# Kernel optimization log

Hardware: AMD Instinct MI355X
Metric: run time of the kernel (lower is better)

The kernel has to match this reference:

```python
import jax, jax.numpy as jnp
import numpy as np

B, S, D = 4, 2048, 768
H = 12
HD = D // H  # 64
EPS = 1e-12  # F.normalize eps


def setup_inputs() -> dict:
    key = jax.random.key(0)
    ks = jax.random.split(key, 6)
    scale = 1.0 / np.sqrt(D)
    x = jax.random.normal(ks[0], (B, S, D), dtype=jnp.float32)
    Wq = jax.random.normal(ks[1], (D, D), dtype=jnp.float32) * scale
    Wk = jax.random.normal(ks[2], (D, D), dtype=jnp.float32) * scale
    Wv = jax.random.normal(ks[3], (D, D), dtype=jnp.float32) * scale
    Wo = jax.random.normal(ks[4], (D, D), dtype=jnp.float32) * scale
    temperature = jnp.ones((H, 1, 1), dtype=jnp.float32)
    return {"x": x, "Wq": Wq, "Wk": Wk, "Wv": Wv, "Wo": Wo, "temperature": temperature}


def _heads(t):
    # [B,S,D] -> [B,H,S,HD]
    return t.reshape(B, S, H, HD).transpose(0, 2, 1, 3)


def reference(x, Wq, Wk, Wv, Wo, temperature):
    # Linear weights stored torch-style [out,in]: y = x @ W.T
    q = _heads(x @ Wq.T)
    k = _heads(x @ Wk.T)
    v = _heads(x @ Wv.T)
    # cosine-sim normalize (F.normalize: x / max(||x||, eps))
    q = q / jnp.maximum(jnp.linalg.norm(q, axis=-1, keepdims=True), EPS)
    k = k / jnp.maximum(jnp.linalg.norm(k, axis=-1, keepdims=True), EPS)
    # [B,H,S,S] scores with per-head learnable temperature
    attn = jnp.einsum("bhqd,bhkd->bhqk", q, k) * temperature  # temperature broadcasts [H,1,1]
    causal = jnp.tril(jnp.ones((S, S), dtype=bool))
    attn = jnp.where(causal, attn, -jnp.inf)
    attn = jax.nn.softmax(attn, axis=-1)
    out = jnp.einsum("bhqk,bhkd->bhqd", attn, v)
    out = out.transpose(0, 2, 1, 3).reshape(B, S, D)
    return out @ Wo.T
```

## Files before the change

### kernel.cpp

```cpp
#include <hip/hip_runtime.h>
#include <hip/hip_bf16.h>

#define B_ 4
#define S_ 2048
#define D_ 768
#define H_ 12
#define HD_ 64
#define M_ (B_*S_)
#define LOG2E 1.44269504088896f

typedef __attribute__((ext_vector_type(8))) short bf8;
typedef __attribute__((ext_vector_type(4))) float f4;
typedef unsigned short u16;
typedef unsigned int   u32;

__device__ __forceinline__ float bf2f(u16 u) {
  union { u32 i; float f; } c; c.i = ((u32)u) << 16; return c.f;
}
__device__ __forceinline__ u16 f2bf(float x) {
  union { float f; u32 i; } c; c.f = x;
  u32 r = (c.i + 0x7FFFu + ((c.i >> 16) & 1u)) >> 16;
  return (u16)r;
}
__device__ __forceinline__ u16 cvt_bf16(float x) {
  u32 r;
  asm("v_cvt_pk_bf16_f32 %0, %1, %1" : "=v"(r) : "v"(x));
  return (u16)r;
}
__device__ __forceinline__ float exp2_raw(float x) {
  float r;
  asm("v_exp_f32 %0, %1" : "=v"(r) : "v"(x));
  return r;
}

__global__ __launch_bounds__(256) void stage_cvt(const float* __restrict__ in,
                                                 u16* __restrict__ out, int n4)
{
  for (int i = blockIdx.x * blockDim.x + threadIdx.x; i < n4; i += gridDim.x * blockDim.x) {
    float4 v = ((const float4*)in)[i];
    ushort4 o;
    o.x = f2bf(v.x); o.y = f2bf(v.y); o.z = f2bf(v.z); o.w = f2bf(v.w);
    ((ushort4*)out)[i] = o;
  }
}

__global__ __launch_bounds__(256) void stage_w4(const float* __restrict__ w0, const float* __restrict__ w1,
                                                const float* __restrict__ w2, const float* __restrict__ w3,
                                                u16* __restrict__ o0, u16* __restrict__ o1,
                                                u16* __restrict__ o2, u16* __restrict__ o3, int n4)
{
  const float* src = (blockIdx.y == 0) ? w0 : (blockIdx.y == 1) ? w1 : (blockIdx.y == 2) ? w2 : w3;
  u16*         dst = (blockIdx.y == 0) ? o0 : (blockIdx.y == 1) ? o1 : (blockIdx.y == 2) ? o2 : o3;
  for (int i = blockIdx.x * blockDim.x + threadIdx.x; i < n4; i += gridDim.x * blockDim.x) {
    float4 v = ((const float4*)src)[i];
    ushort4 o;
    o.x = f2bf(v.x); o.y = f2bf(v.y); o.z = f2bf(v.z); o.w = f2bf(v.w);
    ((ushort4*)dst)[i] = o;
  }
}

__device__ __forceinline__ bf8 ldcvt8(const float* __restrict__ p) {
  float4 a = *(const float4*)p;
  float4 b = *(const float4*)(p + 4);
  bf8 r;
  r[0] = f2bf(a.x); r[1] = f2bf(a.y); r[2] = f2bf(a.z); r[3] = f2bf(a.w);
  r[4] = f2bf(b.x); r[5] = f2bf(b.y); r[6] = f2bf(b.z); r[7] = f2bf(b.w);
  return r;
}

#define MFMA_BF16 __builtin_amdgcn_mfma_f32_16x16x32_bf16

template <int EPI>
__global__ __launch_bounds__(256) void gemm_v2(const u16* __restrict__ A,
                                               const u16* __restrict__ W,
                                               u16* __restrict__ Cb,
                                               float* __restrict__ Cf,
                                               const float* __restrict__ temp)
{
  const int w  = threadIdx.x >> 6;
  const int ln = threadIdx.x & 63;
  const int li = ln & 15, g = ln >> 4;
  const int wr = w >> 1, wc = w & 1;
  const int row0 = blockIdx.x * 64;
  const int col0 = blockIdx.y * 128;

  __shared__ __align__(16) u16 a_lds[64][72];
  __shared__ __align__(16) u16 b_lds[128][72];

  const int rowA = threadIdx.x >> 2;
  const int cA   = (threadIdx.x & 3) * 8;
  const int rowB = threadIdx.x >> 1;
  const int cB   = (threadIdx.x & 1) * 32;

  const u16* Asrc = A + (size_t)(row0 + rowA) * 768 + cA;
  const u16* Bsrc = W + (size_t)(col0 + rowB) * 768 + cB;

  bf8 ra0 = *(const bf8*)(Asrc);
  bf8 ra1 = *(const bf8*)(Asrc + 32);
  bf8 rb0 = *(const bf8*)(Bsrc);
  bf8 rb1 = *(const bf8*)(Bsrc + 8);
  bf8 rb2 = *(const bf8*)(Bsrc + 16);
  bf8 rb3 = *(const bf8*)(Bsrc + 24);

  f4 acc[2][4];
#pragma unroll
  for (int i = 0; i < 2; ++i)
#pragma unroll
    for (int j = 0; j < 4; ++j) acc[i][j] = (f4){0.f, 0.f, 0.f, 0.f};

  for (int kt = 0; kt < 12; ++kt) {
    __syncthreads();
    *(bf8*)&a_lds[rowA][cA]      = ra0;
    *(bf8*)&a_lds[rowA][cA + 32] = ra1;
    *(bf8*)&b_lds[rowB][cB]      = rb0;
    *(bf8*)&b_lds[rowB][cB + 8]  = rb1;
    *(bf8*)&b_lds[rowB][cB + 16] = rb2;
    *(bf8*)&b_lds[rowB][cB + 24] = rb3;
    if (kt < 11) {
      const u16* as = Asrc + (kt + 1) * 64;
      const u16* bs = Bsrc + (kt + 1) * 64;
      ra0 = *(const bf8*)(as);
      ra1 = *(const bf8*)(as + 32);
      rb0 = *(const bf8*)(bs);
      rb1 = *(const bf8*)(bs + 8);
      rb2 = *(const bf8*)(bs + 16);
      rb3 = *(const bf8*)(bs + 24);
    }
    asm volatile("s_waitcnt lgkmcnt(0)" ::: "memory");
    __builtin_amdgcn_s_barrier();

#pragma unroll
    for (int kk = 0; kk < 2; ++kk) {
      bf8 a0 = *(const bf8*)&a_lds[wr * 32 + li][kk * 32 + g * 8];
      bf8 a1 = *(const bf8*)&a_lds[wr * 32 + 16 + li][kk * 32 + g * 8];
      bf8 b0 = *(const bf8*)&b_lds[wc * 64 + li][kk * 32 + g * 8];
      bf8 b1 = *(const bf8*)&b_lds[wc * 64 + 16 + li][kk * 32 + g * 8];
      bf8 b2 = *(const bf8*)&b_lds[wc * 64 + 32 + li][kk * 32 + g * 8];
      bf8 b3 = *(const bf8*)&b_lds[wc * 64 + 48 + li][kk * 32 + g * 8];
      acc[0][0] = MFMA_BF16(a0, b0, acc[0][0], 0, 0, 0);
      acc[0][1] = MFMA_BF16(a0, b1, acc[0][1], 0, 0, 0);
      acc[0][2] = MFMA_BF16(a0, b2, acc[0][2], 0, 0, 0);
      acc[0][3] = MFMA_BF16(a0, b3, acc[0][3], 0, 0, 0);
      acc[1][0] = MFMA_BF16(a1, b0, acc[1][0], 0, 0, 0);
      acc[1][1] = MFMA_BF16(a1, b1, acc[1][1], 0, 0, 0);
      acc[1][2] = MFMA_BF16(a1, b2, acc[1][2], 0, 0, 0);
      acc[1][3] = MFMA_BF16(a1, b3, acc[1][3], 0, 0, 0);
    }
  }

  const int wrow0 = row0 + wr * 32;
  const int wcol0 = col0 + wc * 64;

  if (EPI == 1 || EPI == 2) {
    float tmul = 1.0f;
    if (EPI == 2) tmul = temp[wcol0 >> 6] * LOG2E;
#pragma unroll
    for (int i = 0; i < 2; ++i)
#pragma unroll
      for (int r = 0; r < 4; ++r) {
        float ss = 0.f;
#pragma unroll
        for (int j = 0; j < 4; ++j) ss += acc[i][j][r] * acc[i][j][r];
#pragma unroll
        for (int msk = 1; msk < 16; msk <<= 1) ss += __shfl_xor(ss, msk, 64);
        float scl = tmul / fmaxf(sqrtf(ss), 1e-12f);
#pragma unroll
        for (int j = 0; j < 4; ++j) acc[i][j][r] *= scl;
      }
  }

#pragma unroll
  for (int i = 0; i < 2; ++i)
#pragma unroll
    for (int j = 0; j < 4; ++j)
#pragma unroll
      for (int r = 0; r < 4; ++r) {
        int row = wrow0 + i * 16 + g * 4 + r;
        int col = wcol0 + j * 16 + li;
        if (EPI == 3) Cf[(size_t)row * 768 + col] = acc[i][j][r];
        else          Cb[(size_t)row * 768 + col] = f2bf(acc[i][j][r]);
      }
}

template <int EPI>
__global__ __launch_bounds__(256) void gemm_wf32(const u16* __restrict__ A,
                                                 const float* __restrict__ W,
                                                 u16* __restrict__ Cb,
                                                 float* __restrict__ Cf,
                                                 const float* __restrict__ temp)
{
  const int w  = threadIdx.x >> 6;
  const int ln = threadIdx.x & 63;
  const int li = ln & 15, g = ln >> 4;
  const int wr = w >> 1, wc = w & 1;
  const int row0 = blockIdx.x * 64 + wr * 32;
  const int col0 = blockIdx.y * 128 + wc * 64;

  const u16*   Ap = A + (size_t)(row0 + li) * 768 + g * 8;
  const float* Wp = W + (size_t)(col0 + li) * 768 + g * 8;

  f4 acc[2][4];
#pragma unroll
  for (int i = 0; i < 2; ++i)
#pragma unroll
    for (int j = 0; j < 4; ++j) acc[i][j] = (f4){0.f, 0.f, 0.f, 0.f};

  for (int k = 0; k < 768; k += 32) {
    bf8 a0 = *(const bf8*)(Ap + k);
    bf8 a1 = *(const bf8*)(Ap + (size_t)16 * 768 + k);
    bf8 b0 = ldcvt8(Wp + k);
    bf8 b1 = ldcvt8(Wp + (size_t)16 * 768 + k);
    bf8 b2 = ldcvt8(Wp + (size_t)32 * 768 + k);
    bf8 b3 = ldcvt8(Wp + (size_t)48 * 768 + k);
    acc[0][0] = MFMA_BF16(a0, b0, acc[0][0], 0, 0, 0);
    acc[0][1] = MFMA_BF16(a0, b1, acc[0][1], 0, 0, 0);
    acc[0][2] = MFMA_BF16(a0, b2, acc[0][2], 0, 0, 0);
    acc[0][3] = MFMA_BF16(a0, b3, acc[0][3], 0, 0, 0);
    acc[1][0] = MFMA_BF16(a1, b0, acc[1][0], 0, 0, 0);
    acc[1][1] = MFMA_BF16(a1, b1, acc[1][1], 0, 0, 0);
    acc[1][2] = MFMA_BF16(a1, b2, acc[1][2], 0, 0, 0);
    acc[1][3] = MFMA_BF16(a1, b3, acc[1][3], 0, 0, 0);
  }

  if (EPI == 1 || EPI == 2) {
    float tmul = 1.0f;
    if (EPI == 2) tmul = temp[col0 >> 6] * LOG2E;
#pragma unroll
    for (int i = 0; i < 2; ++i)
#pragma unroll
      for (int r = 0; r < 4; ++r) {
        float ss = 0.f;
#pragma unroll
        for (int j = 0; j < 4; ++j) ss += acc[i][j][r] * acc[i][j][r];
#pragma unroll
        for (int msk = 1; msk < 16; msk <<= 1) ss += __shfl_xor(ss, msk, 64);
        float scl = tmul / fmaxf(sqrtf(ss), 1e-12f);
#pragma unroll
        for (int j = 0; j < 4; ++j) acc[i][j][r] *= scl;
      }
  }

#pragma unroll
  for (int i = 0; i < 2; ++i)
#pragma unroll
    for (int j = 0; j < 4; ++j)
#pragma unroll
      for (int r = 0; r < 4; ++r) {
        int row = row0 + i * 16 + g * 4 + r;
        int col = col0 + j * 16 + li;
        if (EPI == 3) Cf[(size_t)row * 768 + col] = acc[i][j][r];
        else          Cb[(size_t)row * 768 + col] = f2bf(acc[i][j][r]);
      }
}

__global__ __launch_bounds__(256, 4) void flash_attn(const u16* __restrict__ Q,
                                                     const u16* __restrict__ K,
                                                     const u16* __restrict__ V,
                                                     u16* __restrict__ O,
                                                     const float* __restrict__ temp)
{
  const int bid = blockIdx.x;
  const int vid = (bid & 7) * 192 + (bid >> 3);
  const int bh  = vid >> 5;
  const int qt  = 31 - (vid & 31);
  const int b = bh / H_, h = bh % H_;
  const size_t base = (size_t)b * S_ * D_ + h * HD_;
  const u16* Qp = Q + base;
  const u16* Kp = K + base;
  const u16* Vp = V + base;
  u16*       Op = O + base;

  const float C2 = fabsf(temp[h]) * LOG2E;

  const int w  = threadIdx.x >> 6;
  const int ln = threadIdx.x & 63;
  const int li = ln & 15, g = ln >> 4;

  __shared__ __align__(16) u16 k_lds[64][72];
  __shared__ __align__(16) u16 vt[64][72];
  __shared__ __align__(16) u16 p_lds[4][16][72];

  const int q0 = qt * 64;
  const int qrow = q0 + w * 16 + li;

  bf8 qf0 = *(const bf8*)(Qp + (size_t)qrow * D_ + g * 8);
  bf8 qf1 = *(const bf8*)(Qp + (size_t)qrow * D_ + 32 + g * 8);

  const int key2 = (threadIdx.x >> 3) * 2;
  const int d0   = (threadIdx.x & 7) * 8;
  const u16* ksrc = Kp + (size_t)key2 * D_ + d0;
  const u16* vsrc = Vp + (size_t)key2 * D_ + d0;

  bf8 ka = *(const bf8*)(ksrc);
  bf8 kb = *(const bf8*)(ksrc + D_);
  bf8 va = *(const bf8*)(vsrc);
  bf8 vb_ = *(const bf8*)(vsrc + D_);

  f4 o[4];
  float lp[4] = {0.f, 0.f, 0.f, 0.f};
#pragma unroll
  for (int c = 0; c < 4; ++c) o[c] = (f4){0.f, 0.f, 0.f, 0.f};

  for (int kt = 0; kt <= qt; ++kt) {
    __syncthreads();
    {
      *(bf8*)&k_lds[key2][d0]     = ka;
      *(bf8*)&k_lds[key2 + 1][d0] = kb;
#pragma unroll
      for (int j = 0; j < 8; ++j) {
        ushort2 pr;
        pr.x = (u16)va[j]; pr.y = (u16)vb_[j];
        *(ushort2*)&vt[d0 + j][key2 ^ d0] = pr;
      }
    }
    if (kt < qt) {
      const u16* ks = ksrc + (size_t)(kt + 1) * 64 * D_;
      const u16* vs = vsrc + (size_t)(kt + 1) * 64 * D_;
      ka  = *(const bf8*)(ks);
      kb  = *(const bf8*)(ks + D_);
      va  = *(const bf8*)(vs);
      vb_ = *(const bf8*)(vs + D_);
    }
    asm volatile("s_waitcnt lgkmcnt(0)" ::: "memory");
    __builtin_amdgcn_s_barrier();

    f4 sc[4];
#pragma unroll
    for (int c = 0; c < 4; ++c) sc[c] = (f4){0.f, 0.f, 0.f, 0.f};
#pragma unroll
    for (int c = 0; c < 4; ++c) {
      bf8 k0 = *(const bf8*)&k_lds[c * 16 + li][g * 8];
      bf8 k1 = *(const bf8*)&k_lds[c * 16 + li][32 + g * 8];
      sc[c] = MFMA_BF16(qf0, k0, sc[c], 0, 0, 0);
      sc[c] = MFMA_BF16(qf1, k1, sc[c], 0, 0, 0);
    }

    if (kt == qt) {
#pragma unroll
      for (int c = 0; c < 4; ++c)
#pragma unroll
        for (int r = 0; r < 4; ++r) {
          int col = kt * 64 + c * 16 + li;
          int row = q0 + w * 16 + g * 4 + r;
          if (col > row) sc[c][r] = -__builtin_inff();
        }
    }

#pragma unroll
    for (int c = 0; c < 4; ++c)
#pragma unroll
      for (int r = 0; r < 4; ++r) {
        float p = exp2_raw(sc[c][r] - C2);
        sc[c][r] = p;
        lp[r] += p;
      }

#pragma unroll
    for (int c = 0; c < 4; ++c)
#pragma unroll
      for (int r = 0; r < 4; ++r)
        p_lds[w][g * 4 + r][(c * 16 + li) ^ (g << 3)] = cvt_bf16(sc[c][r]);

#pragma unroll
    for (int ks = 0; ks < 2; ++ks) {
      bf8 pa = *(const bf8*)&p_lds[w][li][(ks * 32 + g * 8) ^ ((li >> 2) << 3)];
#pragma unroll
      for (int c = 0; c < 4; ++c) {
        int d  = c * 16 + li;
        int kbx = (ks * 32 + g * 8) ^ (d & 56);
        bf8 vv = *(const bf8*)&vt[d][kbx];
        o[c] = MFMA_BF16(pa, vv, o[c], 0, 0, 0);
      }
    }
  }

  float l[4];
#pragma unroll
  for (int r = 0; r < 4; ++r) {
    float s = lp[r];
#pragma unroll
    for (int msk = 1; msk < 16; msk <<= 1) s += __shfl_xor(s, msk, 64);
    l[r] = 1.0f / s;
  }
#pragma unroll
  for (int c = 0; c < 4; ++c)
#pragma unroll
    for (int r = 0; r < 4; ++r) {
      int row = q0 + w * 16 + g * 4 + r;
      Op[(size_t)row * D_ + c * 16 + li] = cvt_bf16(o[c][r] * l[r]);
    }
}

extern "C" void kernel_launch(void* const* d_in, const int* in_sizes, int n_in,
                              void* d_out, int out_size, void* d_ws, size_t ws_size,
                              hipStream_t stream) {
  const void *xv, *Wqv, *Wkv, *Wvv, *Wov, *tv;
  if (in_sizes[0] == M_ * D_) {
    xv = d_in[0]; Wqv = d_in[1]; Wkv = d_in[2]; Wvv = d_in[3]; Wov = d_in[4]; tv = d_in[5];
  } else {
    Wkv = d_in[0]; Wov = d_in[1]; Wqv = d_in[2]; Wvv = d_in[3]; tv = d_in[4]; xv = d_in[5];
  }
  const float* x    = (const float*)xv;
  const float* Wq   = (const float*)Wqv;
  const float* Wk   = (const float*)Wkv;
  const float* Wv   = (const float*)Wvv;
  const float* Wo   = (const float*)Wov;
  const float* temp = (const float*)tv;

  const size_t SZ  = (size_t)M_ * D_;
  const size_t WSZ = (size_t)D_ * D_;
  u16* ws = (u16*)d_ws;
  u16* Qb = ws;
  u16* Kb = ws + SZ;
  u16* Vb = ws + 2 * SZ;
  u16* XB = (u16*)d_out;

  const bool stageW = ws_size >= (3 * SZ + 4 * WSZ) * sizeof(u16);
  u16* Wqb = ws + 3 * SZ;
  u16* Wkb = Wqb + WSZ;
  u16* Wvb = Wkb + WSZ;
  u16* Wob = Wvb + WSZ;

  stage_cvt<<<2048, 256, 0, stream>>>(x, XB, (int)(SZ / 4));

  dim3 gg(M_ / 64, D_ / 128), bb(256);
  if (stageW) {
    stage_w4<<<dim3(192, 4), 256, 0, stream>>>(Wq, Wk, Wv, Wo, Wqb, Wkb, Wvb, Wob, (int)(WSZ / 4));
    gemm_v2<2><<<gg, bb, 0, stream>>>(XB, Wqb, Qb, nullptr, temp);
    gemm_v2<1><<<gg, bb, 0, stream>>>(XB, Wkb, Kb, nullptr, temp);
    gemm_v2<0><<<gg, bb, 0, stream>>>(XB, Wvb, Vb, nullptr, temp);
  } else {
    gemm_wf32<2><<<gg, bb, 0, stream>>>(XB, Wq, Qb, nullptr, temp);
    gemm_wf32<1><<<gg, bb, 0, stream>>>(XB, Wk, Kb, nullptr, temp);
    gemm_wf32<0><<<gg, bb, 0, stream>>>(XB, Wv, Vb, nullptr, temp);
  }

  flash_attn<<<1536, 256, 0, stream>>>(Qb, Kb, Vb, Qb, temp);

  if (stageW) gemm_v2<3><<<gg, bb, 0, stream>>>(Qb, Wob, nullptr, (float*)d_out, temp);
  else        gemm_wf32<3><<<gg, bb, 0, stream>>>(Qb, Wo, nullptr, (float*)d_out, temp);
}
```

Measured before the change: 154.2 us.

## Use direct global-to-LDS loads with XOR swizzle and merge stage/QKV launches

```diff
diff --git a/kernel.cpp b/kernel.cpp
--- a/kernel.cpp
+++ b/kernel.cpp
@@ -14,6 +14,9 @@
 typedef unsigned short u16;
 typedef unsigned int   u32;
 
+typedef __attribute__((address_space(3))) u32 lds_u32;
+typedef __attribute__((address_space(1))) const u32 glob_u32;
+
 __device__ __forceinline__ float bf2f(u16 u) {
   union { u32 i; float f; } c; c.i = ((u32)u) << 16; return c.f;
 }
@@ -31,6 +34,29 @@
   float r;
   asm("v_exp_f32 %0, %1" : "=v"(r) : "v"(x));
   return r;
+}
+__device__ __forceinline__ void glds16(const u16* g, u16* l) {
+  __builtin_amdgcn_global_load_lds((glob_u32*)g, (lds_u32*)l, 16, 0, 0);
+}
+
+__global__ __launch_bounds__(256) void stage_all(const float* __restrict__ x,
+                                                 const float* __restrict__ w0, const float* __restrict__ w1,
+                                                 const float* __restrict__ w2, const float* __restrict__ w3,
+                                                 u16* __restrict__ xo,
+                                                 u16* __restrict__ o0, u16* __restrict__ o1,
+                                                 u16* __restrict__ o2, u16* __restrict__ o3,
+                                                 int nx4, int nw4)
+{
+  int y = blockIdx.y;
+  const float* src = (y == 0) ? x : (y == 1) ? w0 : (y == 2) ? w1 : (y == 3) ? w2 : w3;
+  u16*         dst = (y == 0) ? xo : (y == 1) ? o0 : (y == 2) ? o1 : (y == 3) ? o2 : o3;
+  int n4 = (y == 0) ? nx4 : nw4;
+  for (int i = blockIdx.x * blockDim.x + threadIdx.x; i < n4; i += gridDim.x * blockDim.x) {
+    float4 v = ((const float4*)src)[i];
+    ushort4 o;
+    o.x = f2bf(v.x); o.y = f2bf(v.y); o.z = f2bf(v.z); o.w = f2bf(v.w);
+    ((ushort4*)dst)[i] = o;
+  }
 }
 
 __global__ __launch_bounds__(256) void stage_cvt(const float* __restrict__ in,
@@ -41,21 +67,6 @@
     ushort4 o;
     o.x = f2bf(v.x); o.y = f2bf(v.y); o.z = f2bf(v.z); o.w = f2bf(v.w);
     ((ushort4*)out)[i] = o;
-  }
-}
-
-__global__ __launch_bounds__(256) void stage_w4(const float* __restrict__ w0, const float* __restrict__ w1,
-                                                const float* __restrict__ w2, const float* __restrict__ w3,
-                                                u16* __restrict__ o0, u16* __restrict__ o1,
-                                                u16* __restrict__ o2, u16* __restrict__ o3, int n4)
-{
-  const float* src = (blockIdx.y == 0) ? w0 : (blockIdx.y == 1) ? w1 : (blockIdx.y == 2) ? w2 : w3;
-  u16*         dst = (blockIdx.y == 0) ? o0 : (blockIdx.y == 1) ? o1 : (blockIdx.y == 2) ? o2 : o3;
-  for (int i = blockIdx.x * blockDim.x + threadIdx.x; i < n4; i += gridDim.x * blockDim.x) {
-    float4 v = ((const float4*)src)[i];
-    ushort4 o;
-    o.x = f2bf(v.x); o.y = f2bf(v.y); o.z = f2bf(v.z); o.w = f2bf(v.w);
-    ((ushort4*)dst)[i] = o;
   }
 }
 
@@ -71,11 +82,12 @@
 #define MFMA_BF16 __builtin_amdgcn_mfma_f32_16x16x32_bf16
 
 template <int EPI>
-__global__ __launch_bounds__(256) void gemm_v2(const u16* __restrict__ A,
-                                               const u16* __restrict__ W,
-                                               u16* __restrict__ Cb,
-                                               float* __restrict__ Cf,
-                                               const float* __restrict__ temp)
+__device__ __forceinline__ void gemm_core(u16* a_lds, u16* b_lds,
+                                          const u16* __restrict__ A,
+                                          const u16* __restrict__ W,
+                                          u16* __restrict__ Cb,
+                                          float* __restrict__ Cf,
+                                          const float* __restrict__ temp)
 {
   const int w  = threadIdx.x >> 6;
   const int ln = threadIdx.x & 63;
@@ -84,23 +96,10 @@
   const int row0 = blockIdx.x * 64;
   const int col0 = blockIdx.y * 128;
 
-  __shared__ __align__(16) u16 a_lds[64][72];
-  __shared__ __align__(16) u16 b_lds[128][72];
-
-  const int rowA = threadIdx.x >> 2;
-  const int cA   = (threadIdx.x & 3) * 8;
-  const int rowB = threadIdx.x >> 1;
-  const int cB   = (threadIdx.x & 1) * 32;
-
-  const u16* Asrc = A + (size_t)(row0 + rowA) * 768 + cA;
-  const u16* Bsrc = W + (size_t)(col0 + rowB) * 768 + cB;
-
-  bf8 ra0 = *(const bf8*)(Asrc);
-  bf8 ra1 = *(const bf8*)(Asrc + 32);
-  bf8 rb0 = *(const bf8*)(Bsrc);
-  bf8 rb1 = *(const bf8*)(Bsrc + 8);
-  bf8 rb2 = *(const bf8*)(Bsrc + 16);
-  bf8 rb3 = *(const bf8*)(Bsrc + 24);
+  const int srow = ln >> 3;
+  const int scol = ((ln & 7) ^ srow) * 8;
+  const u16* Abase = A + (size_t)(row0 + srow) * 768 + scol;
+  const u16* Bbase = W + (size_t)(col0 + srow) * 768 + scol;
 
   f4 acc[2][4];
 #pragma unroll
@@ -109,34 +108,29 @@
     for (int j = 0; j < 4; ++j) acc[i][j] = (f4){0.f, 0.f, 0.f, 0.f};
 
   for (int kt = 0; kt < 12; ++kt) {
+    const int k0 = kt * 64;
+#pragma unroll
+    for (int i = 0; i < 2; ++i) {
+      int seg = w * 2 + i;
+      glds16(Abase + (size_t)(seg * 8) * 768 + k0, a_lds + seg * 512);
+    }
+#pragma unroll
+    for (int i = 0; i < 4; ++i) {
+      int seg = w * 4 + i;
+      glds16(Bbase + (size_t)(seg * 8) * 768 + k0, b_lds + seg * 512);
+    }
+    asm volatile("s_waitcnt vmcnt(0)" ::: "memory");
     __syncthreads();
-    *(bf8*)&a_lds[rowA][cA]      = ra0;
-    *(bf8*)&a_lds[rowA][cA + 32] = ra1;
-    *(bf8*)&b_lds[rowB][cB]      = rb0;
-    *(bf8*)&b_lds[rowB][cB + 8]  = rb1;
-    *(bf8*)&b_lds[rowB][cB + 16] = rb2;
-    *(bf8*)&b_lds[rowB][cB + 24] = rb3;
-    if (kt < 11) {
-      const u16* as = Asrc + (kt + 1) * 64;
-      const u16* bs = Bsrc + (kt + 1) * 64;
-      ra0 = *(const bf8*)(as);
-      ra1 = *(const bf8*)(as + 32);
-      rb0 = *(const bf8*)(bs);
-      rb1 = *(const bf8*)(bs + 8);
-      rb2 = *(const bf8*)(bs + 16);
-      rb3 = *(const bf8*)(bs + 24);
-    }
-    asm volatile("s_waitcnt lgkmcnt(0)" ::: "memory");
-    __builtin_amdgcn_s_barrier();
 
 #pragma unroll
     for (int kk = 0; kk < 2; ++kk) {
-      bf8 a0 = *(const bf8*)&a_lds[wr * 32 + li][kk * 32 + g * 8];
-      bf8 a1 = *(const bf8*)&a_lds[wr * 32 + 16 + li][kk * 32 + g * 8];
-      bf8 b0 = *(const bf8*)&b_lds[wc * 64 + li][kk * 32 + g * 8];
-      bf8 b1 = *(const bf8*)&b_lds[wc * 64 + 16 + li][kk * 32 + g * 8];
-      bf8 b2 = *(const bf8*)&b_lds[wc * 64 + 32 + li][kk * 32 + g * 8];
-      bf8 b3 = *(const bf8*)&b_lds[wc * 64 + 48 + li][kk * 32 + g * 8];
+      const int co = (((kk * 4 + g) ^ (li & 7)) * 8);
+      bf8 a0 = *(const bf8*)(a_lds + (wr * 32 + li) * 64 + co);
+      bf8 a1 = *(const bf8*)(a_lds + (wr * 32 + 16 + li) * 64 + co);
+      bf8 b0 = *(const bf8*)(b_lds + (wc * 64 + li) * 64 + co);
+      bf8 b1 = *(const bf8*)(b_lds + (wc * 64 + 16 + li) * 64 + co);
+      bf8 b2 = *(const bf8*)(b_lds + (wc * 64 + 32 + li) * 64 + co);
+      bf8 b3 = *(const bf8*)(b_lds + (wc * 64 + 48 + li) * 64 + co);
       acc[0][0] = MFMA_BF16(a0, b0, acc[0][0], 0, 0, 0);
       acc[0][1] = MFMA_BF16(a0, b1, acc[0][1], 0, 0, 0);
       acc[0][2] = MFMA_BF16(a0, b2, acc[0][2], 0, 0, 0);
@@ -146,6 +140,7 @@
       acc[1][2] = MFMA_BF16(a1, b2, acc[1][2], 0, 0, 0);
       acc[1][3] = MFMA_BF16(a1, b3, acc[1][3], 0, 0, 0);
     }
+    __syncthreads();
   }
 
   const int wrow0 = row0 + wr * 32;
@@ -180,6 +175,29 @@
         if (EPI == 3) Cf[(size_t)row * 768 + col] = acc[i][j][r];
         else          Cb[(size_t)row * 768 + col] = f2bf(acc[i][j][r]);
       }
+}
+
+__global__ __launch_bounds__(256) void gemm_qkv(const u16* __restrict__ XB,
+                                                const u16* __restrict__ Wq, const u16* __restrict__ Wk,
+                                                const u16* __restrict__ Wv,
+                                                u16* __restrict__ Qb, u16* __restrict__ Kb,
+                                                u16* __restrict__ Vb,
+                                                const float* __restrict__ temp)
+{
+  __shared__ __align__(16) u16 a_lds[64 * 64];
+  __shared__ __align__(16) u16 b_lds[128 * 64];
+  if (blockIdx.z == 0)      gemm_core<2>(a_lds, b_lds, XB, Wq, Qb, nullptr, temp);
+  else if (blockIdx.z == 1) gemm_core<1>(a_lds, b_lds, XB, Wk, Kb, nullptr, temp);
+  else                      gemm_core<0>(a_lds, b_lds, XB, Wv, Vb, nullptr, temp);
+}
+
+__global__ __launch_bounds__(256) void gemm_out(const u16* __restrict__ A,
+                                                const u16* __restrict__ W,
+                                                float* __restrict__ Cf)
+{
+  __shared__ __align__(16) u16 a_lds[64 * 64];
+  __shared__ __align__(16) u16 b_lds[128 * 64];
+  gemm_core<3>(a_lds, b_lds, A, W, nullptr, Cf, nullptr);
 }
 
 template <int EPI>
@@ -421,22 +439,21 @@
   u16* Wvb = Wkb + WSZ;
   u16* Wob = Wvb + WSZ;
 
-  stage_cvt<<<2048, 256, 0, stream>>>(x, XB, (int)(SZ / 4));
-
-  dim3 gg(M_ / 64, D_ / 128), bb(256);
   if (stageW) {
-    stage_w4<<<dim3(192, 4), 256, 0, stream>>>(Wq, Wk, Wv, Wo, Wqb, Wkb, Wvb, Wob, (int)(WSZ / 4));
-    gemm_v2<2><<<gg, bb, 0, stream>>>(XB, Wqb, Qb, nullptr, temp);
-    gemm_v2<1><<<gg, bb, 0, stream>>>(XB, Wkb, Kb, nullptr, temp);
-    gemm_v2<0><<<gg, bb, 0, stream>>>(XB, Wvb, Vb, nullptr, temp);
+    stage_all<<<dim3(512, 5), 256, 0, stream>>>(x, Wq, Wk, Wv, Wo,
+                                                XB, Wqb, Wkb, Wvb, Wob,
+                                                (int)(SZ / 4), (int)(WSZ / 4));
+    gemm_qkv<<<dim3(M_ / 64, D_ / 128, 3), 256, 0, stream>>>(XB, Wqb, Wkb, Wvb,
+                                                             Qb, Kb, Vb, temp);
+    flash_attn<<<1536, 256, 0, stream>>>(Qb, Kb, Vb, Qb, temp);
+    gemm_out<<<dim3(M_ / 64, D_ / 128), 256, 0, stream>>>(Qb, Wob, (float*)d_out);
   } else {
+    dim3 gg(M_ / 64, D_ / 128), bb(256);
+    stage_cvt<<<2048, 256, 0, stream>>>(x, XB, (int)(SZ / 4));
     gemm_wf32<2><<<gg, bb, 0, stream>>>(XB, Wq, Qb, nullptr, temp);
     gemm_wf32<1><<<gg, bb, 0, stream>>>(XB, Wk, Kb, nullptr, temp);
     gemm_wf32<0><<<gg, bb, 0, stream>>>(XB, Wv, Vb, nullptr, temp);
-  }
-
-  flash_attn<<<1536, 256, 0, stream>>>(Qb, Kb, Vb, Qb, temp);
-
-  if (stageW) gemm_v2<3><<<gg, bb, 0, stream>>>(Qb, Wob, nullptr, (float*)d_out, temp);
-  else        gemm_wf32<3><<<gg, bb, 0, stream>>>(Qb, Wo, nullptr, (float*)d_out, temp);
-}
+    flash_attn<<<1536, 256, 0, stream>>>(Qb, Kb, Vb, Qb, temp);
+    gemm_wf32<3><<<gg, bb, 0, stream>>>(Qb, Wo, nullptr, (float*)d_out, temp);
+  }
+}
```

New measurement: 137.0 us. -11.1%, faster.
